# Kernel tuning notes

Measured on AMD Instinct MI355X. Metric: run time of the kernel, lower is better.

Reference implementation:

```python
import jax, jax.numpy as jnp
import numpy as np

TEMPERATURE = 0.1
EPS = 1e-8  # torch cosine_similarity default eps


def _similarity_matrix(left, right):
    # C[i, j] = cosine_similarity(left[i], right[j]) with torch-style eps clamp
    ln = jnp.linalg.norm(left, axis=-1)   # [B]
    rn = jnp.linalg.norm(right, axis=-1)  # [B]
    dots = left @ right.T                 # [B, B]
    denom = jnp.maximum(ln[:, None] * rn[None, :], EPS)
    cos = dots / denom
    # Original builds only the strict upper triangle + diagonal of C, then
    # mirrors the upper triangle: S = triu(C, 1) + diag(C) + triu(C, 1).T
    upper = jnp.triu(cos, k=1)
    return upper + jnp.diag(jnp.diag(cos)) + upper.T


def reference(left_features, right_features):
    sims = _similarity_matrix(left_features, right_features) / TEMPERATURE
    # cross_entropy(sims, eye) == mean_i( -log_softmax(sims)[i, i] )
    logp = jax.nn.log_softmax(sims, axis=-1)
    return -jnp.mean(jnp.diagonal(logp))


def setup_inputs() -> dict:
    key = jax.random.key(0)
    k1, k2 = jax.random.split(key)
    B, D = 4096, 1024
    return {
        "left_features": jax.random.normal(k1, (B, D), dtype=jnp.float32),
        "right_features": jax.random.normal(k2, (B, D), dtype=jnp.float32),
    }
```

## Files before the change

kernel.cpp:

```cpp
#include <hip/hip_runtime.h>

typedef unsigned short u16;
typedef __bf16 bf16x8 __attribute__((ext_vector_type(8)));
typedef float f32x4 __attribute__((ext_vector_type(4)));

#define B_DIM 4096
#define D_DIM 1024
#define TT    64
#define NT    16
#define NSLOT 130

#define GLOAD_LDS16(g, l)                                            \
    __builtin_amdgcn_global_load_lds(                                \
        (const __attribute__((address_space(1))) void*)(g),          \
        (__attribute__((address_space(3))) void*)(l), 16, 0, 0)

__device__ inline u16 f2bf(float f) {
    union { float f; unsigned u; } x; x.f = f;
    unsigned u = x.u;
    return (u16)((u + 0x7fffu + ((u >> 16) & 1u)) >> 16);
}

__global__ __launch_bounds__(256) void norm_convert_kernel(
        const float* __restrict__ L, const float* __restrict__ R,
        u16* __restrict__ Lbf, u16* __restrict__ Rbf,
        float* __restrict__ ln, float* __restrict__ rn) {
    const int wave = threadIdx.x >> 6;
    const int lane = threadIdx.x & 63;
    int g = blockIdx.x * 4 + wave;
    const float* in; u16* outb; float* nout; int row;
    if (g < B_DIM) { in = L; outb = Lbf; nout = ln; row = g; }
    else           { in = R; outb = Rbf; nout = rn; row = g - B_DIM; }

    const float4* r4 = reinterpret_cast<const float4*>(in + (size_t)row * D_DIM);
    ushort4* o4 = reinterpret_cast<ushort4*>(outb + (size_t)row * D_DIM);
    float ss = 0.f;
    #pragma unroll
    for (int c = 0; c < 4; ++c) {
        float4 v = r4[lane + 64 * c];
        ss += v.x * v.x + v.y * v.y + v.z * v.z + v.w * v.w;
        ushort4 o;
        o.x = f2bf(v.x); o.y = f2bf(v.y); o.z = f2bf(v.z); o.w = f2bf(v.w);
        o4[lane + 64 * c] = o;
    }
    #pragma unroll
    for (int off = 32; off > 0; off >>= 1) ss += __shfl_xor(ss, off);
    if (lane == 0) nout[row] = sqrtf(ss);
}

__global__ __launch_bounds__(256, 4) void gemm_fused_kernel(
        const u16* __restrict__ Lbf, const u16* __restrict__ Rbf,
        const float* __restrict__ ln, const float* __restrict__ rn,
        float* __restrict__ part, float* __restrict__ diag) {
    __shared__ __align__(16) u16 Ls[2][64 * 64];
    __shared__ __align__(16) u16 Rs[2][64 * 64];

    int bid = (int)blockIdx.x;
    int swz = (bid & 7) * 260 + (bid >> 3);
    int b = swz, ti = 0;
    while (b >= TT - ti) { b -= TT - ti; ++ti; }
    const int tj = ti + b;
    const int brow = ti * 64, bcol = tj * 64;
    const bool diagblk = (ti == tj);

    const int tid  = threadIdx.x;
    const int lane = tid & 63;
    const int wave = tid >> 6;
    const int wr   = wave >> 1;
    const int wc   = wave & 1;
    const int fr   = lane & 15;

    const int l8 = lane >> 3;
    const int c8 = lane & 7;
    size_t gA[2], gB[2];
    int ldsOff[2];
    #pragma unroll
    for (int s = 0; s < 2; ++s) {
        int row = wave * 16 + s * 8 + l8;
        int chunk = c8 ^ l8;
        gA[s] = (size_t)(brow + row) * D_DIM + chunk * 8;
        gB[s] = (size_t)(bcol + row) * D_DIM + chunk * 8;
        ldsOff[s] = (wave * 16 + s * 8) * 64;
    }

#define STAGE(buf, k0)                                               \
    do {                                                             \
        _Pragma("unroll")                                            \
        for (int s = 0; s < 2; ++s) {                                \
            GLOAD_LDS16(Lbf + gA[s] + (k0), &Ls[buf][ldsOff[s]]);    \
            GLOAD_LDS16(Rbf + gB[s] + (k0), &Rs[buf][ldsOff[s]]);    \
        }                                                            \
    } while (0)

    f32x4 acc[2][2] = {};

#define COMPUTE(buf)                                                  \
    do {                                                              \
        _Pragma("unroll")                                             \
        for (int kk = 0; kk < 2; ++kk) {                              \
            bf16x8 af[2], bfr[2];                                     \
            _Pragma("unroll")                                         \
            for (int m = 0; m < 2; ++m) {                             \
                int row = wr * 32 + m * 16 + fr;                      \
                int cs = ((kk << 2) | (lane >> 4)) ^ (row & 7);       \
                af[m] = *reinterpret_cast<const bf16x8*>(             \
                    &Ls[buf][row * 64 + cs * 8]);                     \
            }                                                         \
            _Pragma("unroll")                                         \
            for (int n = 0; n < 2; ++n) {                             \
                int row = wc * 32 + n * 16 + fr;                      \
                int cs = ((kk << 2) | (lane >> 4)) ^ (row & 7);       \
                bfr[n] = *reinterpret_cast<const bf16x8*>(            \
                    &Rs[buf][row * 64 + cs * 8]);                     \
            }                                                         \
            _Pragma("unroll")                                         \
            for (int m = 0; m < 2; ++m)                               \
                _Pragma("unroll")                                     \
                for (int n = 0; n < 2; ++n)                           \
                    acc[m][n] = __builtin_amdgcn_mfma_f32_16x16x32_bf16( \
                        af[m], bfr[n], acc[m][n], 0, 0, 0);           \
        }                                                             \
    } while (0)

    STAGE(0, 0);

    int cur = 0;
    for (int t = 0; t < NT; ++t) {
        if (t + 1 < NT) {
            STAGE(cur ^ 1, (t + 1) * 64);
            asm volatile("s_waitcnt vmcnt(4)" ::: "memory");
        } else {
            asm volatile("s_waitcnt vmcnt(0)" ::: "memory");
        }
        __builtin_amdgcn_s_barrier();
        asm volatile("" ::: "memory");
        COMPUTE(cur);
        asm volatile("" ::: "memory");
        __builtin_amdgcn_s_barrier();
        cur ^= 1;
    }

    const int fcol  = lane & 15;
    const int frow0 = (lane >> 4) * 4;

    float rnj[2];
    #pragma unroll
    for (int n = 0; n < 2; ++n)
        rnj[n] = rn[bcol + wc * 32 + n * 16 + fcol];

    float colacc[2] = {0.f, 0.f};

    #pragma unroll
    for (int m = 0; m < 2; ++m) {
        #pragma unroll
        for (int r = 0; r < 4; ++r) {
            const int i = brow + wr * 32 + m * 16 + frow0 + r;
            const float lni = ln[i];
            float rowacc = 0.f;
            #pragma unroll
            for (int n = 0; n < 2; ++n) {
                const int j = bcol + wc * 32 + n * 16 + fcol;
                const float denom = fmaxf(lni * rnj[n], 1e-8f);
                const float v = acc[m][n][r] * 10.0f / denom;
                if (diagblk && i == j) diag[i] = v;
                const float e = __expf(v);
                if (i <= j) rowacc += e;
                if (i < j)  colacc[n] += e;
            }
            rowacc += __shfl_xor(rowacc, 1);
            rowacc += __shfl_xor(rowacc, 2);
            rowacc += __shfl_xor(rowacc, 4);
            rowacc += __shfl_xor(rowacc, 8);
            if (fcol == 0) part[(size_t)(2 * tj + wc) * B_DIM + i] = rowacc;
        }
    }
    #pragma unroll
    for (int n = 0; n < 2; ++n) {
        float c = colacc[n];
        c += __shfl_xor(c, 16);
        c += __shfl_xor(c, 32);
        if (lane < 16) {
            const int j = bcol + wc * 32 + n * 16 + fcol;
            const int slot = diagblk ? (128 + wr) : (2 * ti + wr);
            part[(size_t)slot * B_DIM + j] = c;
        }
    }
#undef STAGE
#undef COMPUTE
}

__global__ __launch_bounds__(256) void loss_stage1_kernel(
        const float* __restrict__ part, const float* __restrict__ diag,
        float* __restrict__ partial) {
    const int i = blockIdx.x * 256 + threadIdx.x;
    float rs = 0.f;
    #pragma unroll 10
    for (int k = 0; k < NSLOT; ++k)
        rs += part[(size_t)k * B_DIM + i];
    float s = logf(rs) - diag[i];
    #pragma unroll
    for (int off = 32; off > 0; off >>= 1) s += __shfl_down(s, off);
    __shared__ float red[4];
    if ((threadIdx.x & 63) == 0) red[threadIdx.x >> 6] = s;
    __syncthreads();
    if (threadIdx.x == 0)
        partial[blockIdx.x] = red[0] + red[1] + red[2] + red[3];
}

__global__ __launch_bounds__(64) void loss_stage2_kernel(
        const float* __restrict__ partial, float* __restrict__ out) {
    float s = (threadIdx.x < 16) ? partial[threadIdx.x] : 0.f;
    #pragma unroll
    for (int off = 8; off > 0; off >>= 1) s += __shfl_down(s, off);
    if (threadIdx.x == 0) out[0] = s / (float)B_DIM;
}

extern "C" void kernel_launch(void* const* d_in, const int* in_sizes, int n_in,
                              void* d_out, int out_size, void* d_ws, size_t ws_size,
                              hipStream_t stream) {
    const float* L = (const float*)d_in[0];
    const float* R = (const float*)d_in[1];

    char* ws = (char*)d_ws;
    size_t o = 0;
    u16* Lbf     = (u16*)(ws + o);   o += (size_t)B_DIM * D_DIM * sizeof(u16);
    u16* Rbf     = (u16*)(ws + o);   o += (size_t)B_DIM * D_DIM * sizeof(u16);
    float* ln    = (float*)(ws + o); o += (size_t)B_DIM * sizeof(float);
    float* rn    = (float*)(ws + o); o += (size_t)B_DIM * sizeof(float);
    float* part  = (float*)(ws + o); o += (size_t)NSLOT * B_DIM * sizeof(float);
    float* diag  = (float*)(ws + o); o += (size_t)B_DIM * sizeof(float);
    float* partial = (float*)(ws + o); o += 16 * sizeof(float);

    norm_convert_kernel<<<2 * B_DIM / 4, 256, 0, stream>>>(L, R, Lbf, Rbf, ln, rn);

    const int nblocks = TT * (TT + 1) / 2;
    gemm_fused_kernel<<<nblocks, 256, 0, stream>>>(Lbf, Rbf, ln, rn, part, diag);

    loss_stage1_kernel<<<16, 256, 0, stream>>>(part, diag, partial);
    loss_stage2_kernel<<<1, 64, 0, stream>>>(partial, (float*)d_out);
}
```

Baseline: 127.1 us.

## Triple-buffer GEMM K-loop and merge loss reduction kernels via atomic counter

The GEMM main loop moves from double to triple buffering of the LDS tiles, prefetching two K-steps ahead with a deeper vmcnt wait. Launch bounds are lowered to 3 blocks per CU to fit the larger shared-memory footprint. Separately, the two final loss kernels are merged into one that uses a last-block-done atomic counter, reset in the norm kernel, which saves one kernel launch. The trade-off is lower occupancy in the GEMM in exchange for more latency hiding per block.

```diff
diff --git a/kernel.cpp b/kernel.cpp
--- a/kernel.cpp
+++ b/kernel.cpp
@@ -9,6 +9,7 @@
 #define TT    64
 #define NT    16
 #define NSLOT 130
+#define NRED  16
 
 #define GLOAD_LDS16(g, l)                                            \
     __builtin_amdgcn_global_load_lds(                                \
@@ -24,7 +25,9 @@
 __global__ __launch_bounds__(256) void norm_convert_kernel(
         const float* __restrict__ L, const float* __restrict__ R,
         u16* __restrict__ Lbf, u16* __restrict__ Rbf,
-        float* __restrict__ ln, float* __restrict__ rn) {
+        float* __restrict__ ln, float* __restrict__ rn,
+        unsigned* __restrict__ counter) {
+    if (blockIdx.x == 0 && threadIdx.x == 0) *counter = 0u;
     const int wave = threadIdx.x >> 6;
     const int lane = threadIdx.x & 63;
     int g = blockIdx.x * 4 + wave;
@@ -48,12 +51,12 @@
     if (lane == 0) nout[row] = sqrtf(ss);
 }
 
-__global__ __launch_bounds__(256, 4) void gemm_fused_kernel(
+__global__ __launch_bounds__(256, 3) void gemm_fused_kernel(
         const u16* __restrict__ Lbf, const u16* __restrict__ Rbf,
         const float* __restrict__ ln, const float* __restrict__ rn,
         float* __restrict__ part, float* __restrict__ diag) {
-    __shared__ __align__(16) u16 Ls[2][64 * 64];
-    __shared__ __align__(16) u16 Rs[2][64 * 64];
+    __shared__ __align__(16) u16 Ls[3][64 * 64];
+    __shared__ __align__(16) u16 Rs[3][64 * 64];
 
     int bid = (int)blockIdx.x;
     int swz = (bid & 7) * 260 + (bid >> 3);
@@ -123,21 +126,23 @@
     } while (0)
 
     STAGE(0, 0);
-
-    int cur = 0;
+    STAGE(1, 64);
+
+    #pragma unroll
     for (int t = 0; t < NT; ++t) {
-        if (t + 1 < NT) {
-            STAGE(cur ^ 1, (t + 1) * 64);
+        if (t + 2 < NT) {
+            STAGE((t + 2) % 3, (t + 2) * 64);
+            asm volatile("s_waitcnt vmcnt(8)" ::: "memory");
+        } else if (t + 1 < NT) {
             asm volatile("s_waitcnt vmcnt(4)" ::: "memory");
         } else {
             asm volatile("s_waitcnt vmcnt(0)" ::: "memory");
         }
         __builtin_amdgcn_s_barrier();
         asm volatile("" ::: "memory");
-        COMPUTE(cur);
+        COMPUTE(t % 3);
         asm volatile("" ::: "memory");
         __builtin_amdgcn_s_barrier();
-        cur ^= 1;
     }
 
     const int fcol  = lane & 15;
@@ -189,9 +194,10 @@
 #undef COMPUTE
 }
 
-__global__ __launch_bounds__(256) void loss_stage1_kernel(
+__global__ __launch_bounds__(256) void loss_final_kernel(
         const float* __restrict__ part, const float* __restrict__ diag,
-        float* __restrict__ partial) {
+        float* __restrict__ scratch, unsigned* __restrict__ counter,
+        float* __restrict__ out) {
     const int i = blockIdx.x * 256 + threadIdx.x;
     float rs = 0.f;
     #pragma unroll 10
@@ -203,16 +209,19 @@
     __shared__ float red[4];
     if ((threadIdx.x & 63) == 0) red[threadIdx.x >> 6] = s;
     __syncthreads();
-    if (threadIdx.x == 0)
-        partial[blockIdx.x] = red[0] + red[1] + red[2] + red[3];
-}
-
-__global__ __launch_bounds__(64) void loss_stage2_kernel(
-        const float* __restrict__ partial, float* __restrict__ out) {
-    float s = (threadIdx.x < 16) ? partial[threadIdx.x] : 0.f;
-    #pragma unroll
-    for (int off = 8; off > 0; off >>= 1) s += __shfl_down(s, off);
-    if (threadIdx.x == 0) out[0] = s / (float)B_DIM;
+    if (threadIdx.x == 0) {
+        scratch[blockIdx.x] = red[0] + red[1] + red[2] + red[3];
+        __threadfence();
+        unsigned prev = atomicAdd(counter, 1u);
+        if (prev == NRED - 1) {
+            __threadfence();
+            volatile float* vs = scratch;
+            float tot = 0.f;
+            #pragma unroll
+            for (int k = 0; k < NRED; ++k) tot += vs[k];
+            out[0] = tot / (float)B_DIM;
+        }
+    }
 }
 
 extern "C" void kernel_launch(void* const* d_in, const int* in_sizes, int n_in,
@@ -229,13 +238,13 @@
     float* rn    = (float*)(ws + o); o += (size_t)B_DIM * sizeof(float);
     float* part  = (float*)(ws + o); o += (size_t)NSLOT * B_DIM * sizeof(float);
     float* diag  = (float*)(ws + o); o += (size_t)B_DIM * sizeof(float);
-    float* partial = (float*)(ws + o); o += 16 * sizeof(float);
-
-    norm_convert_kernel<<<2 * B_DIM / 4, 256, 0, stream>>>(L, R, Lbf, Rbf, ln, rn);
+    float* scratch = (float*)(ws + o); o += NRED * sizeof(float);
+    unsigned* counter = (unsigned*)(ws + o); o += sizeof(unsigned);
+
+    norm_convert_kernel<<<2 * B_DIM / 4, 256, 0, stream>>>(L, R, Lbf, Rbf, ln, rn, counter);
 
     const int nblocks = TT * (TT + 1) / 2;
     gemm_fused_kernel<<<nblocks, 256, 0, stream>>>(Lbf, Rbf, ln, rn, part, diag);
 
-    loss_stage1_kernel<<<16, 256, 0, stream>>>(part, diag, partial);
-    loss_stage2_kernel<<<1, 64, 0, stream>>>(partial, (float*)d_out);
-}
+    loss_final_kernel<<<NRED, 256, 0, stream>>>(part, diag, scratch, counter, (float*)d_out);
+}
```

New measurement: 127.7 us. About the same (+0.5%).
